# Optimization experiments

Hardware: AMD Instinct MI355X
Metric: run time of the kernel (lower is better)

Reference implementation:

```python
import jax, jax.numpy as jnp
import numpy as np

N = 100000
E = 800000
D = 128


def setup_inputs() -> dict:
    key = jax.random.key(0)
    k1, k2, k3, k4 = jax.random.split(key, 4)
    x = jax.random.normal(k1, (N, D), dtype=jnp.float32)
    edge_index = jax.random.randint(k2, (2, E), 0, N, dtype=jnp.int64)
    s = 1.0 / np.sqrt(D)
    W1 = jax.random.uniform(k3, (D, D), jnp.float32, -s, s)
    b1 = jnp.zeros((D,), jnp.float32)
    W2 = jax.random.uniform(k4, (D, D), jnp.float32, -s, s)
    b2 = jnp.zeros((D,), jnp.float32)
    return {"x": x, "edge_index": edge_index, "W1": W1, "b1": b1, "W2": W2, "b2": b2}


def _degree(idx, n, dtype):
    return jax.ops.segment_sum(jnp.ones(idx.shape, dtype), idx, num_segments=n)


def _graph_conv(x, row, col, W, b, residual, act):
    n = x.shape[0]
    deg_out = jnp.clip(_degree(row, n, x.dtype), 1.0)          # [N]
    x_src = x * jax.lax.rsqrt(deg_out)[:, None]                # [N, D]
    # scatter-add messages from source (row) into target (col)
    agg = jax.ops.segment_sum(x_src[row], col, num_segments=n)  # [N, D]
    out = agg @ W.T + b
    deg_in = jnp.clip(_degree(col, n, x.dtype), 1.0)
    out = out * jax.lax.rsqrt(deg_in)[:, None]
    if residual:
        out = out + x  # res_fc is Identity (in_dim == out_dim)
    if act:
        out = jax.nn.relu(out)
    return out


def reference(x, edge_index, W1, b1, W2, b2):
    row, col = edge_index[0], edge_index[1]
    # layer 1: relu + residual; layer 2 (last, encoding=False): no act, no residual
    h = _graph_conv(x, row, col, W1, b1, residual=True, act=True)
    h = _graph_conv(h, row, col, W2, b2, residual=False, act=False)
    return h
```

## Files before the change

### kernel.cpp

```cpp
#include <hip/hip_runtime.h>


#define NN 100000
#define EE 800000
#define DD 128
#define NB1 98
#define NTILE (NN / 16)

#define CC 64
#define CH (EE / CC)
#define HALF 50000
#define HWORDS 12500
#define NWORDS 25000

typedef __attribute__((ext_vector_type(8))) short short8;
typedef __attribute__((ext_vector_type(4))) float floatx4;

__device__ inline float bf2f(unsigned int u16) {
    union { unsigned int i; float f; } c;
    c.i = u16 << 16;
    return c.f;
}
__device__ inline ushort f2bf(float f) {
    union { float f; unsigned int i; } c;
    c.f = f;
    unsigned int u = c.i;
    return (ushort)((u + 0x7fffu + ((u >> 16) & 1u)) >> 16);
}

__global__ __launch_bounds__(512) void count_kernel(const int* __restrict__ row,
                                                    const int* __restrict__ col,
                                                    unsigned int* __restrict__ partial_out,
                                                    unsigned int* __restrict__ partial_in,
                                                    unsigned char* __restrict__ off_u8) {
    __shared__ unsigned int h[HWORDS];
    for (int i = threadIdx.x; i < HWORDS; i += 512) h[i] = 0;
    __syncthreads();

    const int kind = blockIdx.x >> 7;
    const int r = (blockIdx.x >> 6) & 1;
    const int c = blockIdx.x & 63;
    const int* __restrict__ idx = kind ? row : col;
    const int base = c * CH;
    const int lo = r * HALF;

    for (int t = threadIdx.x; t < CH; t += 512) {
        const int e = base + t;
        const unsigned int d = (unsigned int)(idx[e] - lo);
        if (d < (unsigned int)HALF) {
            const int sh = 8 * (d & 3);
            unsigned int old = atomicAdd(&h[d >> 2], 1u << sh);
            if (kind == 0) off_u8[e] = (unsigned char)((old >> sh) & 0xffu);
        }
    }
    __syncthreads();

    unsigned int* dst = (kind ? partial_out : partial_in) + c * NWORDS + r * HWORDS;
    for (int i = threadIdx.x; i < HWORDS; i += 512) dst[i] = h[i];
}

__global__ __launch_bounds__(256) void node_kernel(const unsigned int* __restrict__ partial_out,
                                                   const unsigned int* __restrict__ partial_in,
                                                   int* __restrict__ cnt_total,
                                                   unsigned int* __restrict__ xoff,
                                                   float* __restrict__ dinv_out,
                                                   float* __restrict__ dinv_in) {
    const int w = blockIdx.x * 256 + threadIdx.x;
    if (w >= NWORDS) return;
    unsigned int prefix = 0;
    unsigned int tot_out = 0;
#pragma unroll
    for (int c = 0; c < CC; ++c) {
        unsigned int v = partial_in[c * NWORDS + w];
        xoff[c * NWORDS + w] = prefix;
        prefix += v;
        tot_out += partial_out[c * NWORDS + w];
    }
    int4 ct;
    float4 fi, fo;
#pragma unroll
    for (int j = 0; j < 4; ++j) {
        int din  = (int)((prefix  >> (8 * j)) & 0xffu);
        int dout = (int)((tot_out >> (8 * j)) & 0xffu);
        ((int*)&ct)[j]   = din;
        ((float*)&fi)[j] = rsqrtf((float)max(din, 1));
        ((float*)&fo)[j] = rsqrtf((float)max(dout, 1));
    }
    ((int4*)cnt_total)[w] = ct;
    ((float4*)dinv_in)[w] = fi;
    ((float4*)dinv_out)[w] = fo;
}

__global__ __launch_bounds__(256) void scan1_kernel(const int* __restrict__ cnt,
                                                    int* __restrict__ excl,
                                                    int* __restrict__ bsums) {
    __shared__ int tmp[256];
    const int t = threadIdx.x;
    const int base = blockIdx.x * 1024 + t * 4;
    int a[4];
#pragma unroll
    for (int q = 0; q < 4; ++q) a[q] = (base + q < NN) ? cnt[base + q] : 0;
    int s = a[0] + a[1] + a[2] + a[3];
    tmp[t] = s;
    __syncthreads();
    for (int off = 1; off < 256; off <<= 1) {
        int v = 0;
        if (t >= off) v = tmp[t - off];
        __syncthreads();
        tmp[t] += v;
        __syncthreads();
    }
    int excl_s = tmp[t] - s;
    if (t == 255) bsums[blockIdx.x] = tmp[t];
    int run = excl_s;
#pragma unroll
    for (int q = 0; q < 4; ++q) {
        if (base + q < NN) excl[base + q] = run;
        run += a[q];
    }
}

__global__ __launch_bounds__(256) void scan2_kernel(int* __restrict__ bsums, int nb) {
    __shared__ int tmp[256];
    const int t = threadIdx.x;
    int s = (t < nb) ? bsums[t] : 0;
    tmp[t] = s;
    __syncthreads();
    for (int off = 1; off < 256; off <<= 1) {
        int v = 0;
        if (t >= off) v = tmp[t - off];
        __syncthreads();
        tmp[t] += v;
        __syncthreads();
    }
    if (t < nb) bsums[t] = tmp[t] - s;
}

__global__ __launch_bounds__(256) void scan3_kernel(const int* __restrict__ excl,
                                                    const int* __restrict__ bsums,
                                                    int* __restrict__ row_start) {
    int i = blockIdx.x * 256 + threadIdx.x;
    if (i < NN) row_start[i] = excl[i] + bsums[i >> 10];
}

__global__ __launch_bounds__(256) void fill_kernel(const int* __restrict__ row,
                                                   const int* __restrict__ col,
                                                   const int* __restrict__ row_start,
                                                   const unsigned char* __restrict__ xoff_u8,
                                                   const unsigned char* __restrict__ off_u8,
                                                   int* __restrict__ srcs) {
    int e = blockIdx.x * 256 + threadIdx.x;
    if (e < EE) {
        const int cl = col[e];
        const int c = e / CH;
        const int pos = row_start[cl] + (int)xoff_u8[(size_t)c * NN + cl] + (int)off_u8[e];
        srcs[pos] = row[e];
    }
}

__global__ __launch_bounds__(256) void prescale_kernel(const float* __restrict__ x,
                                                       const float* __restrict__ dinv_out,
                                                       ushort* __restrict__ xb) {
    int idx = blockIdx.x * 256 + threadIdx.x;
    if (idx >= NN * 32) return;
    int n = idx >> 5;
    float s = dinv_out[n];
    float4 v = ((const float4*)x)[idx];
    ushort4 o;
    o.x = f2bf(v.x * s);
    o.y = f2bf(v.y * s);
    o.z = f2bf(v.z * s);
    o.w = f2bf(v.w * s);
    ((ushort4*)xb)[idx] = o;
}

__global__ __launch_bounds__(256) void gather_kernel(const ushort* __restrict__ src,
                                                     const int* __restrict__ row_start,
                                                     const int* __restrict__ srcs,
                                                     ushort* __restrict__ agg) {
    const int node = blockIdx.x * 16 + (threadIdx.x >> 4);
    const int lane = threadIdx.x & 15;
    if (node >= NN) return;
    int p = row_start[node];
    const int end = (node + 1 < NN) ? row_start[node + 1] : EE;
    float a0 = 0.f, a1 = 0.f, a2 = 0.f, a3 = 0.f;
    float a4 = 0.f, a5 = 0.f, a6 = 0.f, a7 = 0.f;

#define ACCUM(V)                                     \
    do {                                             \
        a0 += bf2f((V).x & 0xffffu);                 \
        a1 += bf2f((V).x >> 16);                     \
        a2 += bf2f((V).y & 0xffffu);                 \
        a3 += bf2f((V).y >> 16);                     \
        a4 += bf2f((V).z & 0xffffu);                 \
        a5 += bf2f((V).z >> 16);                     \
        a6 += bf2f((V).w & 0xffffu);                 \
        a7 += bf2f((V).w >> 16);                     \
    } while (0)

    for (; p + 3 < end; p += 4) {
        int s0 = srcs[p];
        int s1 = srcs[p + 1];
        int s2 = srcs[p + 2];
        int s3 = srcs[p + 3];
        uint4 v0 = ((const uint4*)(src + (size_t)s0 * DD))[lane];
        uint4 v1 = ((const uint4*)(src + (size_t)s1 * DD))[lane];
        uint4 v2 = ((const uint4*)(src + (size_t)s2 * DD))[lane];
        uint4 v3 = ((const uint4*)(src + (size_t)s3 * DD))[lane];
        ACCUM(v0); ACCUM(v1); ACCUM(v2); ACCUM(v3);
    }
    for (; p < end; ++p) {
        int s0 = srcs[p];
        uint4 v0 = ((const uint4*)(src + (size_t)s0 * DD))[lane];
        ACCUM(v0);
    }
#undef ACCUM

    uint4 o;
    o.x = (unsigned int)f2bf(a0) | ((unsigned int)f2bf(a1) << 16);
    o.y = (unsigned int)f2bf(a2) | ((unsigned int)f2bf(a3) << 16);
    o.z = (unsigned int)f2bf(a4) | ((unsigned int)f2bf(a5) << 16);
    o.w = (unsigned int)f2bf(a6) | ((unsigned int)f2bf(a7) << 16);
    ((uint4*)(agg + (size_t)node * DD))[lane] = o;
}

template <bool L1>
__global__ __launch_bounds__(256) void gemm_ep(const ushort* __restrict__ agg,
                                               const float* __restrict__ W,
                                               const float* __restrict__ bias,
                                               const float* __restrict__ dinv_in,
                                               const float* __restrict__ dinv_out,
                                               const float* __restrict__ x,
                                               ushort* __restrict__ hs,
                                               float* __restrict__ out) {
    __shared__ ushort Ws[128 * 136];
    {
        int j = threadIdx.x >> 1;
        int k0 = (threadIdx.x & 1) * 64;
        const float4* wp = (const float4*)(W + (size_t)j * DD + k0);
        ushort* dst = Ws + j * 136 + k0;
#pragma unroll
        for (int q = 0; q < 16; ++q) {
            float4 v = wp[q];
            ushort4 o;
            o.x = f2bf(v.x); o.y = f2bf(v.y); o.z = f2bf(v.z); o.w = f2bf(v.w);
            *(ushort4*)(dst + q * 4) = o;
        }
    }
    __syncthreads();

    const int wave = threadIdx.x >> 6;
    const int lane = threadIdx.x & 63;
    const int tile = blockIdx.x * 4 + wave;
    if (tile >= NTILE) return;
    const int mi = lane & 15;
    const int quad = lane >> 4;
    const int m0 = tile * 16;

    floatx4 acc[8];
#pragma unroll
    for (int t = 0; t < 8; ++t) acc[t] = (floatx4){0.f, 0.f, 0.f, 0.f};

    const ushort* ap = agg + (size_t)(m0 + mi) * DD + quad * 8;
#pragma unroll
    for (int s = 0; s < 4; ++s) {
        short8 a = *(const short8*)(ap + s * 32);
#pragma unroll
        for (int t = 0; t < 8; ++t) {
            short8 b = *(const short8*)(Ws + (t * 16 + mi) * 136 + s * 32 + quad * 8);
            acc[t] = __builtin_amdgcn_mfma_f32_16x16x32_bf16(a, b, acc[t], 0, 0, 0);
        }
    }

    float dv[4], dov[4];
#pragma unroll
    for (int i = 0; i < 4; ++i) {
        int r = m0 + quad * 4 + i;
        dv[i] = dinv_in[r];
        if (L1) dov[i] = dinv_out[r];
    }
#pragma unroll
    for (int t = 0; t < 8; ++t) {
        int c = t * 16 + mi;
        float bv = bias[c];
#pragma unroll
        for (int i = 0; i < 4; ++i) {
            int r = m0 + quad * 4 + i;
            float o = (acc[t][i] + bv) * dv[i];
            if (L1) {
                o += x[(size_t)r * DD + c];
                o = fmaxf(o, 0.f);
                hs[(size_t)r * DD + c] = f2bf(o * dov[i]);
            } else {
                out[(size_t)r * DD + c] = o;
            }
        }
    }
}

extern "C" void kernel_launch(void* const* d_in, const int* in_sizes, int n_in,
                              void* d_out, int out_size, void* d_ws, size_t ws_size,
                              hipStream_t stream) {
    const float* x  = (const float*)d_in[0];
    const int*   ei = (const int*)d_in[1];
    const float* W1 = (const float*)d_in[2];
    const float* b1 = (const float*)d_in[3];
    const float* W2 = (const float*)d_in[4];
    const float* b2 = (const float*)d_in[5];
    float* out = (float*)d_out;

    const int* row = ei;
    const int* col = ei + EE;

    ushort* agg     = (ushort*)d_ws;
    ushort* xb      = agg + (size_t)NN * DD;
    float* dinv_out = (float*)(xb + (size_t)NN * DD);
    float* dinv_in  = dinv_out + NN;
    int*   cnt      = (int*)(dinv_in + NN);
    int*   excl     = cnt + NN;
    int*   row_st   = excl + NN;
    int*   srcs     = row_st + NN;
    int*   bsums    = srcs + EE;

    unsigned char* off_u8      = (unsigned char*)agg;
    unsigned int*  partial_in  = (unsigned int*)(off_u8 + EE);
    unsigned int*  partial_out = partial_in + CC * NWORDS;
    unsigned int*  xoff        = partial_out + CC * NWORDS;

    count_kernel<<<256, 512, 0, stream>>>(row, col, partial_out, partial_in, off_u8);
    node_kernel<<<(NWORDS + 255) / 256, 256, 0, stream>>>(partial_out, partial_in, cnt, xoff,
                                                          dinv_out, dinv_in);
    scan1_kernel<<<NB1, 256, 0, stream>>>(cnt, excl, bsums);
    scan2_kernel<<<1, 256, 0, stream>>>(bsums, NB1);
    scan3_kernel<<<(NN + 255) / 256, 256, 0, stream>>>(excl, bsums, row_st);
    fill_kernel<<<(EE + 255) / 256, 256, 0, stream>>>(row, col, row_st,
                                                      (const unsigned char*)xoff, off_u8, srcs);

    prescale_kernel<<<(NN * 32 + 255) / 256, 256, 0, stream>>>(x, dinv_out, xb);
    gather_kernel<<<(NN + 15) / 16, 256, 0, stream>>>(xb, row_st, srcs, agg);
    gemm_ep<true><<<(NTILE + 3) / 4, 256, 0, stream>>>(agg, W1, b1, dinv_in, dinv_out, x,
                                                       xb, nullptr);

    gather_kernel<<<(NN + 15) / 16, 256, 0, stream>>>(xb, row_st, srcs, agg);
    gemm_ep<false><<<(NTILE + 3) / 4, 256, 0, stream>>>(agg, W2, b2, dinv_in, nullptr, nullptr,
                                                        nullptr, out);
}
```

Before: 280.9 us.

## Fold scan3 into consumers, preconvert weights to bf16, unroll gather by 8

Removes the scan3 launch by having fill and gather compute row starts from excl plus block sums directly. Adds a small kernel that converts W1 and W2 to bf16 once, so each GEMM block no longer converts the weights into shared memory and waits at a barrier; B fragments are now read from global or L1 instead. Adds an 8-way unrolled edge loop in gather to keep more loads in flight. Reading B from global instead of LDS may add cache traffic, and the extra unroll raises register use.

```diff
diff --git a/kernel.cpp b/kernel.cpp
--- a/kernel.cpp
+++ b/kernel.cpp
@@ -136,16 +136,11 @@
     if (t < nb) bsums[t] = tmp[t] - s;
 }
 
-__global__ __launch_bounds__(256) void scan3_kernel(const int* __restrict__ excl,
-                                                    const int* __restrict__ bsums,
-                                                    int* __restrict__ row_start) {
-    int i = blockIdx.x * 256 + threadIdx.x;
-    if (i < NN) row_start[i] = excl[i] + bsums[i >> 10];
-}
 
 __global__ __launch_bounds__(256) void fill_kernel(const int* __restrict__ row,
                                                    const int* __restrict__ col,
-                                                   const int* __restrict__ row_start,
+                                                   const int* __restrict__ excl,
+                                                   const int* __restrict__ bsums,
                                                    const unsigned char* __restrict__ xoff_u8,
                                                    const unsigned char* __restrict__ off_u8,
                                                    int* __restrict__ srcs) {
@@ -153,8 +148,8 @@
     if (e < EE) {
         const int cl = col[e];
         const int c = e / CH;
-        const int pos = row_start[cl] + (int)xoff_u8[(size_t)c * NN + cl] + (int)off_u8[e];
-        srcs[pos] = row[e];
+        const int rs = excl[cl] + bsums[cl >> 10];
+        srcs[rs + (int)xoff_u8[(size_t)c * NN + cl] + (int)off_u8[e]] = row[e];
     }
 }
 
@@ -174,15 +169,31 @@
     ((ushort4*)xb)[idx] = o;
 }
 
+__global__ __launch_bounds__(256) void wconv_kernel(const float* __restrict__ W1,
+                                                    const float* __restrict__ W2,
+                                                    ushort* __restrict__ wb1,
+                                                    ushort* __restrict__ wb2) {
+    int i = blockIdx.x * 256 + threadIdx.x;
+    if (i >= 8192) return;
+    const float* W = (i < 4096) ? W1 : W2;
+    ushort* wb = (i < 4096) ? wb1 : wb2;
+    int j = i & 4095;
+    float4 v = ((const float4*)W)[j];
+    ushort4 o;
+    o.x = f2bf(v.x); o.y = f2bf(v.y); o.z = f2bf(v.z); o.w = f2bf(v.w);
+    ((ushort4*)wb)[j] = o;
+}
+
 __global__ __launch_bounds__(256) void gather_kernel(const ushort* __restrict__ src,
-                                                     const int* __restrict__ row_start,
+                                                     const int* __restrict__ excl,
+                                                     const int* __restrict__ bsums,
                                                      const int* __restrict__ srcs,
                                                      ushort* __restrict__ agg) {
     const int node = blockIdx.x * 16 + (threadIdx.x >> 4);
     const int lane = threadIdx.x & 15;
     if (node >= NN) return;
-    int p = row_start[node];
-    const int end = (node + 1 < NN) ? row_start[node + 1] : EE;
+    int p = excl[node] + bsums[node >> 10];
+    const int end = (node + 1 < NN) ? excl[node + 1] + bsums[(node + 1) >> 10] : EE;
     float a0 = 0.f, a1 = 0.f, a2 = 0.f, a3 = 0.f;
     float a4 = 0.f, a5 = 0.f, a6 = 0.f, a7 = 0.f;
 
@@ -198,6 +209,26 @@
         a7 += bf2f((V).w >> 16);                     \
     } while (0)
 
+    for (; p + 7 < end; p += 8) {
+        int s0 = srcs[p];
+        int s1 = srcs[p + 1];
+        int s2 = srcs[p + 2];
+        int s3 = srcs[p + 3];
+        int s4 = srcs[p + 4];
+        int s5 = srcs[p + 5];
+        int s6 = srcs[p + 6];
+        int s7 = srcs[p + 7];
+        uint4 v0 = ((const uint4*)(src + (size_t)s0 * DD))[lane];
+        uint4 v1 = ((const uint4*)(src + (size_t)s1 * DD))[lane];
+        uint4 v2 = ((const uint4*)(src + (size_t)s2 * DD))[lane];
+        uint4 v3 = ((const uint4*)(src + (size_t)s3 * DD))[lane];
+        uint4 v4 = ((const uint4*)(src + (size_t)s4 * DD))[lane];
+        uint4 v5 = ((const uint4*)(src + (size_t)s5 * DD))[lane];
+        uint4 v6 = ((const uint4*)(src + (size_t)s6 * DD))[lane];
+        uint4 v7 = ((const uint4*)(src + (size_t)s7 * DD))[lane];
+        ACCUM(v0); ACCUM(v1); ACCUM(v2); ACCUM(v3);
+        ACCUM(v4); ACCUM(v5); ACCUM(v6); ACCUM(v7);
+    }
     for (; p + 3 < end; p += 4) {
         int s0 = srcs[p];
         int s1 = srcs[p + 1];
@@ -226,29 +257,13 @@
 
 template <bool L1>
 __global__ __launch_bounds__(256) void gemm_ep(const ushort* __restrict__ agg,
-                                               const float* __restrict__ W,
+                                               const ushort* __restrict__ wb,
                                                const float* __restrict__ bias,
                                                const float* __restrict__ dinv_in,
                                                const float* __restrict__ dinv_out,
                                                const float* __restrict__ x,
                                                ushort* __restrict__ hs,
                                                float* __restrict__ out) {
-    __shared__ ushort Ws[128 * 136];
-    {
-        int j = threadIdx.x >> 1;
-        int k0 = (threadIdx.x & 1) * 64;
-        const float4* wp = (const float4*)(W + (size_t)j * DD + k0);
-        ushort* dst = Ws + j * 136 + k0;
-#pragma unroll
-        for (int q = 0; q < 16; ++q) {
-            float4 v = wp[q];
-            ushort4 o;
-            o.x = f2bf(v.x); o.y = f2bf(v.y); o.z = f2bf(v.z); o.w = f2bf(v.w);
-            *(ushort4*)(dst + q * 4) = o;
-        }
-    }
-    __syncthreads();
-
     const int wave = threadIdx.x >> 6;
     const int lane = threadIdx.x & 63;
     const int tile = blockIdx.x * 4 + wave;
@@ -262,12 +277,13 @@
     for (int t = 0; t < 8; ++t) acc[t] = (floatx4){0.f, 0.f, 0.f, 0.f};
 
     const ushort* ap = agg + (size_t)(m0 + mi) * DD + quad * 8;
+    const ushort* bp = wb + (size_t)mi * DD + quad * 8;
 #pragma unroll
     for (int s = 0; s < 4; ++s) {
         short8 a = *(const short8*)(ap + s * 32);
 #pragma unroll
         for (int t = 0; t < 8; ++t) {
-            short8 b = *(const short8*)(Ws + (t * 16 + mi) * 136 + s * 32 + quad * 8);
+            short8 b = *(const short8*)(bp + (size_t)t * 16 * DD + s * 32);
             acc[t] = __builtin_amdgcn_mfma_f32_16x16x32_bf16(a, b, acc[t], 0, 0, 0);
         }
     }
@@ -318,30 +334,31 @@
     float* dinv_in  = dinv_out + NN;
     int*   cnt      = (int*)(dinv_in + NN);
     int*   excl     = cnt + NN;
-    int*   row_st   = excl + NN;
-    int*   srcs     = row_st + NN;
+    int*   srcs     = excl + NN;
     int*   bsums    = srcs + EE;
+    ushort* wb1     = (ushort*)(bsums + 256);
+    ushort* wb2     = wb1 + DD * DD;
 
     unsigned char* off_u8      = (unsigned char*)agg;
     unsigned int*  partial_in  = (unsigned int*)(off_u8 + EE);
     unsigned int*  partial_out = partial_in + CC * NWORDS;
     unsigned int*  xoff        = partial_out + CC * NWORDS;
 
+    wconv_kernel<<<32, 256, 0, stream>>>(W1, W2, wb1, wb2);
     count_kernel<<<256, 512, 0, stream>>>(row, col, partial_out, partial_in, off_u8);
     node_kernel<<<(NWORDS + 255) / 256, 256, 0, stream>>>(partial_out, partial_in, cnt, xoff,
                                                           dinv_out, dinv_in);
     scan1_kernel<<<NB1, 256, 0, stream>>>(cnt, excl, bsums);
     scan2_kernel<<<1, 256, 0, stream>>>(bsums, NB1);
-    scan3_kernel<<<(NN + 255) / 256, 256, 0, stream>>>(excl, bsums, row_st);
-    fill_kernel<<<(EE + 255) / 256, 256, 0, stream>>>(row, col, row_st,
+    fill_kernel<<<(EE + 255) / 256, 256, 0, stream>>>(row, col, excl, bsums,
                                                       (const unsigned char*)xoff, off_u8, srcs);
 
     prescale_kernel<<<(NN * 32 + 255) / 256, 256, 0, stream>>>(x, dinv_out, xb);
-    gather_kernel<<<(NN + 15) / 16, 256, 0, stream>>>(xb, row_st, srcs, agg);
-    gemm_ep<true><<<(NTILE + 3) / 4, 256, 0, stream>>>(agg, W1, b1, dinv_in, dinv_out, x,
+    gather_kernel<<<(NN + 15) / 16, 256, 0, stream>>>(xb, excl, bsums, srcs, agg);
+    gemm_ep<true><<<(NTILE + 3) / 4, 256, 0, stream>>>(agg, wb1, b1, dinv_in, dinv_out, x,
                                                        xb, nullptr);
 
-    gather_kernel<<<(NN + 15) / 16, 256, 0, stream>>>(xb, row_st, srcs, agg);
-    gemm_ep<false><<<(NTILE + 3) / 4, 256, 0, stream>>>(agg, W2, b2, dinv_in, nullptr, nullptr,
+    gather_kernel<<<(NN + 15) / 16, 256, 0, stream>>>(xb, excl, bsums, srcs, agg);
+    gemm_ep<false><<<(NTILE + 3) / 4, 256, 0, stream>>>(agg, wb2, b2, dinv_in, nullptr, nullptr,
                                                         nullptr, out);
 }
```

Measured after the change: 305.0 us. 8.6% more time.
